# Kernel tuning notes

Measured on AMD Instinct MI355X. Metric: run time of the kernel, lower is better.

## Reference

```python
import jax, jax.numpy as jnp
import numpy as np

B, C, H, W, D = 4, 64, 64, 192, 24


def setup_inputs() -> dict:
    key = jax.random.key(0)
    ks = jax.random.split(key, 8)
    x = jax.random.normal(ks[0], (B, C, H, W), dtype=jnp.float32)
    y = jax.random.normal(ks[1], (B, C, H, W), dtype=jnp.float32)
    # disparity coordinate samples: pixel x-coordinates in [0, W-1]
    d1 = jax.random.uniform(ks[2], (B, D, H, W), dtype=jnp.float32) * (W - 1.0)
    d2 = jax.random.uniform(ks[3], (B, D, H, W), dtype=jnp.float32) * (W - 1.0)
    s = 1.0 / np.sqrt(C)
    qw = jax.random.normal(ks[4], (C, C), dtype=jnp.float32) * s
    qb = jax.random.normal(ks[5], (C,), dtype=jnp.float32) * 0.01
    kw = jax.random.normal(ks[6], (C, C), dtype=jnp.float32) * s
    kb = jax.random.normal(ks[7], (C,), dtype=jnp.float32) * 0.01
    return {"x": x, "y": y, "disp_range_samples1": d1, "disp_range_samples2": d2,
            "ndisp": D, "qw": qw, "qb": qb, "kw": kw, "kb": kb}


def _conv1x1(x, w, b):
    return jnp.einsum('oi,bihw->bohw', w, x) + b[None, :, None, None]


def _cost_volume(Q, K, disp_x):
    """mean_c( Q * grid_sample(K, bilinear, zeros, align_corners=False) ).
    Q,K: [B,C,H,W]; disp_x: [B,D,H,W] pixel x-coords. Returns [B,D,H,W]."""
    b, c, h, w = K.shape
    # torch grid_sample(align_corners=False) unnormalization of
    # coords = pix/((dim-1)/2)-1  ->  pix*dim/(dim-1) - 0.5
    xs = disp_x * (w / (w - 1.0)) - 0.5                      # [B,D,H,W]
    ys_row = jnp.arange(h, dtype=xs.dtype) * (h / (h - 1.0)) - 0.5
    ys = jnp.broadcast_to(ys_row[None, None, :, None], xs.shape)
    x0 = jnp.floor(xs)
    y0 = jnp.floor(ys)
    tx = xs - x0
    ty = ys - y0
    x0i = x0.astype(jnp.int32)
    y0i = y0.astype(jnp.int32)

    def corner(dy, dx, wgt):
        yi = y0i + dy
        xi = x0i + dx
        valid = ((yi >= 0) & (yi < h) & (xi >= 0) & (xi < w)).astype(Q.dtype)
        yc = jnp.clip(yi, 0, h - 1)
        xc = jnp.clip(xi, 0, w - 1)
        # per-batch gather: [C,H,W] indexed by [D,H,W] -> [C,D,H,W]
        g = jax.vmap(lambda im, yy, xx: im[:, yy, xx])(K, yc, xc)  # [B,C,D,H,W]
        return jnp.einsum('bchw,bcdhw->bdhw', Q, g * (wgt * valid)[:, None])

    cost = (corner(0, 0, (1.0 - ty) * (1.0 - tx)) +
            corner(0, 1, (1.0 - ty) * tx) +
            corner(1, 0, ty * (1.0 - tx)) +
            corner(1, 1, ty * tx))
    return cost / c


def reference(x, y, disp_range_samples1, disp_range_samples2, ndisp, qw, qb, kw, kb):
    assert ndisp == disp_range_samples1.shape[1]
    Q1 = _conv1x1(x, qw, qb)
    K1 = _conv1x1(y, kw, kb)
    cost1 = _cost_volume(Q1, K1, disp_range_samples1)
    Q2 = _conv1x1(y, qw, qb)
    K2 = _conv1x1(x, kw, kb)
    cost2 = _cost_volume(Q2, K2, disp_range_samples2)
    return (cost1, cost2)
```

## Files before the change

kernel.cpp:

```cpp
#include <hip/hip_runtime.h>
#include <stdint.h>

#define BB 4
#define CC 64
#define HH 64
#define WW 192
#define DD 24
#define HWQ (HH * WW)
#define PIX (BB * HWQ)

typedef __attribute__((ext_vector_type(8))) short short8;
typedef __attribute__((ext_vector_type(4))) float floatx4;

__device__ __forceinline__ float bf1(uint16_t u) {
    union { uint32_t i; float f; } c; c.i = ((uint32_t)u) << 16; return c.f;
}
__device__ __forceinline__ uint16_t f2bf(float f) {
    union { float f; uint32_t i; } c; c.f = f;
    uint32_t u = c.i;
    return (uint16_t)((u + 0x7fffu + ((u >> 16) & 1u)) >> 16);
}

#define A_SHORTS ((size_t)2 * PIX * CC)
#define S_F32OFF 4240

__global__ __launch_bounds__(64) void prep_kernel(
    const float* __restrict__ qw, const float* __restrict__ qb,
    const float* __restrict__ kw, const float* __restrict__ kb,
    float* __restrict__ fws) {
    const int bid = blockIdx.x;
    const int j   = threadIdx.x;
    if (bid < 64) {
        float acc = 0.f;
        for (int c = 0; c < CC; c++)
            acc = fmaf(qw[c * CC + bid], kw[c * CC + j], acc);
        fws[bid * 64 + j] = acc;
    } else if (bid == 64) {
        float bt = 0.f;
        for (int c = 0; c < CC; c++) bt = fmaf(qb[c], kw[c * CC + j], bt);
        fws[4096 + j] = bt;
        if (j == 0) {
            float g = 0.f;
            for (int c = 0; c < CC; c++) g = fmaf(qb[c], kb[c], g);
            fws[4224] = g;
        }
    } else {
        float al = 0.f;
        for (int c = 0; c < CC; c++) al = fmaf(qw[c * CC + j], kb[c], al);
        fws[4160 + j] = al;
    }
}

__global__ __launch_bounds__(256) void convA_kernel(
    const float* __restrict__ x, const float* __restrict__ y,
    const float* __restrict__ fws, uint16_t* __restrict__ A) {
    const int v = blockIdx.y;
    const float* src = v ? y : x;
    const float* G     = fws;
    const float* beta  = fws + 4096;
    const float* alpha = fws + 4160;
    const float* gamma = fws + 4224;
    float* s = const_cast<float*>(fws) + S_F32OFF;

    __shared__ float wt[64][64];
    __shared__ float bs[64], al[64];
    __shared__ float gm;
    const int tid = threadIdx.y * 64 + threadIdx.x;
    for (int idx = tid; idx < 4096; idx += 256) wt[idx >> 6][idx & 63] = G[idx];
    if (tid < 64) { bs[tid] = beta[tid]; al[tid] = alpha[tid]; }
    if (tid == 64) gm = *gamma;
    __syncthreads();

    const int pix0 = blockIdx.x * 256 + threadIdx.x * 4;
    const int b    = pix0 / HWQ;
    const int hw0  = pix0 - b * HWQ;
    const int j0   = threadIdx.y * 16;

    float acc[4][16];
#pragma unroll
    for (int p = 0; p < 4; p++)
#pragma unroll
        for (int k = 0; k < 16; k++) acc[p][k] = bs[j0 + k];
    float sac[4] = {gm, gm, gm, gm};

    const float* sp = src + (size_t)b * CC * HWQ + hw0;
#pragma unroll 4
    for (int i = 0; i < 64; i++) {
        float4 raw = *reinterpret_cast<const float4*>(sp + (size_t)i * HWQ);
        const float* wr = &wt[i][j0];
        const float av = al[i];
        sac[0] = fmaf(raw.x, av, sac[0]);
        sac[1] = fmaf(raw.y, av, sac[1]);
        sac[2] = fmaf(raw.z, av, sac[2]);
        sac[3] = fmaf(raw.w, av, sac[3]);
#pragma unroll
        for (int k = 0; k < 16; k++) {
            float wv = wr[k];
            acc[0][k] = fmaf(raw.x, wv, acc[0][k]);
            acc[1][k] = fmaf(raw.y, wv, acc[1][k]);
            acc[2][k] = fmaf(raw.z, wv, acc[2][k]);
            acc[3][k] = fmaf(raw.w, wv, acc[3][k]);
        }
    }

    uint16_t* dstv = A + (size_t)v * PIX * CC;
#pragma unroll
    for (int p = 0; p < 4; p++) {
        uint32_t pk[8];
#pragma unroll
        for (int k = 0; k < 8; k++)
            pk[k] = (uint32_t)f2bf(acc[p][2 * k]) | ((uint32_t)f2bf(acc[p][2 * k + 1]) << 16);
        uint16_t* dp = dstv + (size_t)(pix0 + p) * CC + j0;
        uint4 lo; lo.x = pk[0]; lo.y = pk[1]; lo.z = pk[2]; lo.w = pk[3];
        uint4 hi; hi.x = pk[4]; hi.y = pk[5]; hi.z = pk[6]; hi.w = pk[7];
        *reinterpret_cast<uint4*>(dp)     = lo;
        *reinterpret_cast<uint4*>(dp + 8) = hi;
    }
    if (threadIdx.y == 0) {
        float4 sv; sv.x = sac[0]; sv.y = sac[1]; sv.z = sac[2]; sv.w = sac[3];
        *reinterpret_cast<float4*>(s + (size_t)v * PIX + pix0) = sv;
    }
}

__global__ __launch_bounds__(256) void cost_kernel(
    const float* __restrict__ x, const float* __restrict__ y,
    const float* __restrict__ disp1, const float* __restrict__ disp2,
    const uint16_t* __restrict__ A, const float* __restrict__ fws,
    float* __restrict__ out) {
    const int h   = blockIdx.x;
    const int b   = blockIdx.y;
    const int v   = blockIdx.z >> 2;
    const int qtr = blockIdx.z & 3;
    const int w0  = qtr * 48;

    const float*    Yv   = v ? x : y;
    const float*    disp = v ? disp2 : disp1;
    const uint16_t* Ab   = A + ((size_t)v * PIX + (size_t)b * HWQ + h * WW + w0) * CC;
    const float*    sb   = fws + S_F32OFF + (size_t)v * PIX + (size_t)b * HWQ + h * WW + w0;

    const float ys  = (float)h * (float)(64.0 / 63.0) - 0.5f;
    const float y0f = floorf(ys);
    const float ty  = ys - y0f;
    const int   y0  = (int)y0f;
    const int   y1  = y0 + 1;
    const float vy0 = (y0 >= 0 && y0 < HH) ? 1.f : 0.f;
    const float vy1 = (y1 >= 0 && y1 < HH) ? 1.f : 0.f;
    const int   y0c = min(max(y0, 0), HH - 1);
    const int   y1c = min(max(y1, 0), HH - 1);
    const float ey0 = (1.f - ty) * vy0;
    const float ey1 = ty * vy1;
    const float eysum = ey0 + ey1;

    __shared__ uint16_t Yc[192 * 68];
    __shared__ uint16_t Pt[48 * 196];

    const int tid  = threadIdx.x;
    const int wave = tid >> 6;
    const int lane = tid & 63;
    const int lq   = lane >> 4;
    const int ln   = lane & 15;

    const uint16_t* ar0 = Ab + (size_t)ln * CC + lq * 8;
    short8 a0 = *reinterpret_cast<const short8*>(ar0);
    short8 a1 = *reinterpret_cast<const short8*>(ar0 + 32);

    const float* Yb0 = Yv + ((size_t)b * CC * HH + y0c) * WW;
    const float* Yb1 = Yv + ((size_t)b * CC * HH + y1c) * WW;
#pragma unroll
    for (int k = 0; k < 12; k++) {
        const int cg = wave + 4 * (k & 3);
        const int xx = (k >> 2) * 64 + lane;
        uint32_t pk[2];
#pragma unroll
        for (int half = 0; half < 2; half++) {
            uint32_t pv = 0;
#pragma unroll
            for (int j = 0; j < 2; j++) {
                const int c = cg * 4 + half * 2 + j;
                const float v0 = Yb0[(size_t)c * HH * WW + xx];
                const float v1 = Yb1[(size_t)c * HH * WW + xx];
                const float cb = fmaf(ey1, v1, ey0 * v0);
                pv |= ((uint32_t)f2bf(cb)) << (16 * j);
            }
            pk[half] = pv;
        }
        *reinterpret_cast<uint2*>(&Yc[xx * 68 + cg * 4]) = *reinterpret_cast<uint2*>(pk);
    }
    __syncthreads();

    for (int ch = 0; ch < 3; ch++) {
        short8 na0 = a0, na1 = a1;
        if (ch < 2) {
            const uint16_t* ar = Ab + (size_t)((ch + 1) * 16 + ln) * CC + lq * 8;
            na0 = *reinterpret_cast<const short8*>(ar);
            na1 = *reinterpret_cast<const short8*>(ar + 32);
        }
#pragma unroll
        for (int t3 = 0; t3 < 3; t3++) {
            const int Rb = (wave * 3 + t3) * 16;
            const uint16_t* yrow = &Yc[(Rb + ln) * 68 + lq * 8];
            short8 b0, b1;
            *reinterpret_cast<uint2*>(&b0)       = *reinterpret_cast<const uint2*>(yrow);
            *(reinterpret_cast<uint2*>(&b0) + 1) = *reinterpret_cast<const uint2*>(yrow + 4);
            *reinterpret_cast<uint2*>(&b1)       = *reinterpret_cast<const uint2*>(yrow + 32);
            *(reinterpret_cast<uint2*>(&b1) + 1) = *reinterpret_cast<const uint2*>(yrow + 36);
            floatx4 acc = {0.f, 0.f, 0.f, 0.f};
            acc = __builtin_amdgcn_mfma_f32_16x16x32_bf16(a0, b0, acc, 0, 0, 0);
            acc = __builtin_amdgcn_mfma_f32_16x16x32_bf16(a1, b1, acc, 0, 0, 0);
            const int pcol = Rb + ln;
            const int wl   = ch * 16 + lq * 4;
            Pt[(wl + 0) * 196 + pcol] = f2bf(acc[0]);
            Pt[(wl + 1) * 196 + pcol] = f2bf(acc[1]);
            Pt[(wl + 2) * 196 + pcol] = f2bf(acc[2]);
            Pt[(wl + 3) * 196 + pcol] = f2bf(acc[3]);
        }
        a0 = na0; a1 = na1;
    }
    __syncthreads();

    const float cx = (float)(192.0 / 191.0);
    const float inv_c = 1.f / 64.f;
    for (int o = tid; o < 48 * DD; o += 256) {
        const int wl = o % 48;
        const int d  = o / 48;
        const int w  = w0 + wl;
        const float dsv = disp[((size_t)(b * DD + d) * HH + h) * WW + w];
        const float xs  = dsv * cx - 0.5f;
        const float x0f = floorf(xs);
        const float tx  = xs - x0f;
        const int   x0  = (int)x0f;
        const int   x1  = x0 + 1;
        const float vx0 = (x0 >= 0 && x0 < WW) ? 1.f : 0.f;
        const float vx1 = (x1 >= 0 && x1 < WW) ? 1.f : 0.f;
        const int   x0c = min(max(x0, 0), WW - 1);
        const int   x1c = min(max(x1, 0), WW - 1);
        const float wx0 = (1.f - tx) * vx0;
        const float wx1 = tx * vx1;
        const float pc0 = bf1(Pt[wl * 196 + x0c]);
        const float pc1 = bf1(Pt[wl * 196 + x1c]);
        const float res = wx0 * pc0 + wx1 * pc1 + sb[wl] * (eysum * (wx0 + wx1));
        out[(((size_t)(v * BB + b) * DD + d) * HH + h) * WW + w] = res * inv_c;
    }
}

extern "C" void kernel_launch(void* const* d_in, const int* in_sizes, int n_in,
                              void* d_out, int out_size, void* d_ws, size_t ws_size,
                              hipStream_t stream) {
    const float* x  = (const float*)d_in[0];
    const float* y  = (const float*)d_in[1];
    const float* d1 = (const float*)d_in[2];
    const float* d2 = (const float*)d_in[3];
    const float* qw = (const float*)d_in[5];
    const float* qb = (const float*)d_in[6];
    const float* kw = (const float*)d_in[7];
    const float* kb = (const float*)d_in[8];

    uint16_t* A   = (uint16_t*)d_ws;
    float*    fws = (float*)((uint16_t*)d_ws + A_SHORTS);
    float*    out = (float*)d_out;

    prep_kernel<<<dim3(66), dim3(64), 0, stream>>>(qw, qb, kw, kb, fws);
    convA_kernel<<<dim3(PIX / 256, 2), dim3(64, 4), 0, stream>>>(x, y, fws, A);
    cost_kernel<<<dim3(HH, BB, 8), dim3(256), 0, stream>>>(x, y, d1, d2, A, fws, out);
}
```

Measured before the change: 138.5 us.

## Process full image row per block with 1024 threads to avoid redundant Yc builds

Each cost block now handles a whole row of 192 query pixels instead of a quarter, using 1024 threads and two halves of 96 pixels each. The bilinearly blended, bf16-packed K row (Yc) is built once per row instead of four times, which cuts the redundant global reads of the input row. The price is fewer, larger blocks (512 instead of 2048), a larger shared-memory tile, extra barriers, and only 12 of the 16 waves doing MFMA work, so occupancy and latency hiding may suffer.

```diff
diff --git a/kernel.cpp b/kernel.cpp
--- a/kernel.cpp
+++ b/kernel.cpp
@@ -122,21 +122,19 @@
     }
 }
 
-__global__ __launch_bounds__(256) void cost_kernel(
+__global__ __launch_bounds__(1024) void cost_kernel(
     const float* __restrict__ x, const float* __restrict__ y,
     const float* __restrict__ disp1, const float* __restrict__ disp2,
     const uint16_t* __restrict__ A, const float* __restrict__ fws,
     float* __restrict__ out) {
-    const int h   = blockIdx.x;
-    const int b   = blockIdx.y;
-    const int v   = blockIdx.z >> 2;
-    const int qtr = blockIdx.z & 3;
-    const int w0  = qtr * 48;
+    const int h = blockIdx.x;
+    const int b = blockIdx.y;
+    const int v = blockIdx.z;
 
     const float*    Yv   = v ? x : y;
     const float*    disp = v ? disp2 : disp1;
-    const uint16_t* Ab   = A + ((size_t)v * PIX + (size_t)b * HWQ + h * WW + w0) * CC;
-    const float*    sb   = fws + S_F32OFF + (size_t)v * PIX + (size_t)b * HWQ + h * WW + w0;
+    const uint16_t* Ab   = A + ((size_t)v * PIX + (size_t)b * HWQ + h * WW) * CC;
+    const float*    sb   = fws + S_F32OFF + (size_t)v * PIX + (size_t)b * HWQ + h * WW;
 
     const float ys  = (float)h * (float)(64.0 / 63.0) - 0.5f;
     const float y0f = floorf(ys);
@@ -152,7 +150,7 @@
     const float eysum = ey0 + ey1;
 
     __shared__ uint16_t Yc[192 * 68];
-    __shared__ uint16_t Pt[48 * 196];
+    __shared__ uint16_t Pt[96 * 196];
 
     const int tid  = threadIdx.x;
     const int wave = tid >> 6;
@@ -160,16 +158,12 @@
     const int lq   = lane >> 4;
     const int ln   = lane & 15;
 
-    const uint16_t* ar0 = Ab + (size_t)ln * CC + lq * 8;
-    short8 a0 = *reinterpret_cast<const short8*>(ar0);
-    short8 a1 = *reinterpret_cast<const short8*>(ar0 + 32);
-
     const float* Yb0 = Yv + ((size_t)b * CC * HH + y0c) * WW;
     const float* Yb1 = Yv + ((size_t)b * CC * HH + y1c) * WW;
 #pragma unroll
-    for (int k = 0; k < 12; k++) {
-        const int cg = wave + 4 * (k & 3);
-        const int xx = (k >> 2) * 64 + lane;
+    for (int k = 0; k < 3; k++) {
+        const int cg = wave;
+        const int xx = k * 64 + lane;
         uint32_t pk[2];
 #pragma unroll
         for (int half = 0; half < 2; half++) {
@@ -188,58 +182,60 @@
     }
     __syncthreads();
 
-    for (int ch = 0; ch < 3; ch++) {
-        short8 na0 = a0, na1 = a1;
-        if (ch < 2) {
-            const uint16_t* ar = Ab + (size_t)((ch + 1) * 16 + ln) * CC + lq * 8;
-            na0 = *reinterpret_cast<const short8*>(ar);
-            na1 = *reinterpret_cast<const short8*>(ar + 32);
-        }
-#pragma unroll
-        for (int t3 = 0; t3 < 3; t3++) {
-            const int Rb = (wave * 3 + t3) * 16;
-            const uint16_t* yrow = &Yc[(Rb + ln) * 68 + lq * 8];
-            short8 b0, b1;
-            *reinterpret_cast<uint2*>(&b0)       = *reinterpret_cast<const uint2*>(yrow);
-            *(reinterpret_cast<uint2*>(&b0) + 1) = *reinterpret_cast<const uint2*>(yrow + 4);
-            *reinterpret_cast<uint2*>(&b1)       = *reinterpret_cast<const uint2*>(yrow + 32);
-            *(reinterpret_cast<uint2*>(&b1) + 1) = *reinterpret_cast<const uint2*>(yrow + 36);
-            floatx4 acc = {0.f, 0.f, 0.f, 0.f};
-            acc = __builtin_amdgcn_mfma_f32_16x16x32_bf16(a0, b0, acc, 0, 0, 0);
-            acc = __builtin_amdgcn_mfma_f32_16x16x32_bf16(a1, b1, acc, 0, 0, 0);
-            const int pcol = Rb + ln;
-            const int wl   = ch * 16 + lq * 4;
-            Pt[(wl + 0) * 196 + pcol] = f2bf(acc[0]);
-            Pt[(wl + 1) * 196 + pcol] = f2bf(acc[1]);
-            Pt[(wl + 2) * 196 + pcol] = f2bf(acc[2]);
-            Pt[(wl + 3) * 196 + pcol] = f2bf(acc[3]);
-        }
-        a0 = na0; a1 = na1;
-    }
-    __syncthreads();
-
     const float cx = (float)(192.0 / 191.0);
     const float inv_c = 1.f / 64.f;
-    for (int o = tid; o < 48 * DD; o += 256) {
-        const int wl = o % 48;
-        const int d  = o / 48;
-        const int w  = w0 + wl;
-        const float dsv = disp[((size_t)(b * DD + d) * HH + h) * WW + w];
-        const float xs  = dsv * cx - 0.5f;
-        const float x0f = floorf(xs);
-        const float tx  = xs - x0f;
-        const int   x0  = (int)x0f;
-        const int   x1  = x0 + 1;
-        const float vx0 = (x0 >= 0 && x0 < WW) ? 1.f : 0.f;
-        const float vx1 = (x1 >= 0 && x1 < WW) ? 1.f : 0.f;
-        const int   x0c = min(max(x0, 0), WW - 1);
-        const int   x1c = min(max(x1, 0), WW - 1);
-        const float wx0 = (1.f - tx) * vx0;
-        const float wx1 = tx * vx1;
-        const float pc0 = bf1(Pt[wl * 196 + x0c]);
-        const float pc1 = bf1(Pt[wl * 196 + x1c]);
-        const float res = wx0 * pc0 + wx1 * pc1 + sb[wl] * (eysum * (wx0 + wx1));
-        out[(((size_t)(v * BB + b) * DD + d) * HH + h) * WW + w] = res * inv_c;
+
+    for (int half = 0; half < 2; half++) {
+        if (wave < 12) {
+            const int mcl = wave >> 1;
+            const uint16_t* ar = Ab + (size_t)(half * 96 + mcl * 16 + ln) * CC + lq * 8;
+            short8 a0 = *reinterpret_cast<const short8*>(ar);
+            short8 a1 = *reinterpret_cast<const short8*>(ar + 32);
+#pragma unroll
+            for (int i = 0; i < 6; i++) {
+                const int nt = (wave & 1) * 6 + i;
+                const int Rb = nt * 16;
+                const uint16_t* yrow = &Yc[(Rb + ln) * 68 + lq * 8];
+                short8 b0, b1;
+                *reinterpret_cast<uint2*>(&b0)       = *reinterpret_cast<const uint2*>(yrow);
+                *(reinterpret_cast<uint2*>(&b0) + 1) = *reinterpret_cast<const uint2*>(yrow + 4);
+                *reinterpret_cast<uint2*>(&b1)       = *reinterpret_cast<const uint2*>(yrow + 32);
+                *(reinterpret_cast<uint2*>(&b1) + 1) = *reinterpret_cast<const uint2*>(yrow + 36);
+                floatx4 acc = {0.f, 0.f, 0.f, 0.f};
+                acc = __builtin_amdgcn_mfma_f32_16x16x32_bf16(a0, b0, acc, 0, 0, 0);
+                acc = __builtin_amdgcn_mfma_f32_16x16x32_bf16(a1, b1, acc, 0, 0, 0);
+                const int pcol = Rb + ln;
+                const int wl   = mcl * 16 + lq * 4;
+                Pt[(wl + 0) * 196 + pcol] = f2bf(acc[0]);
+                Pt[(wl + 1) * 196 + pcol] = f2bf(acc[1]);
+                Pt[(wl + 2) * 196 + pcol] = f2bf(acc[2]);
+                Pt[(wl + 3) * 196 + pcol] = f2bf(acc[3]);
+            }
+        }
+        __syncthreads();
+
+        for (int o = tid; o < 96 * DD; o += 1024) {
+            const int wl = o % 96;
+            const int d  = o / 96;
+            const int w  = half * 96 + wl;
+            const float dsv = disp[((size_t)(b * DD + d) * HH + h) * WW + w];
+            const float xs  = dsv * cx - 0.5f;
+            const float x0f = floorf(xs);
+            const float tx  = xs - x0f;
+            const int   x0  = (int)x0f;
+            const int   x1  = x0 + 1;
+            const float vx0 = (x0 >= 0 && x0 < WW) ? 1.f : 0.f;
+            const float vx1 = (x1 >= 0 && x1 < WW) ? 1.f : 0.f;
+            const int   x0c = min(max(x0, 0), WW - 1);
+            const int   x1c = min(max(x1, 0), WW - 1);
+            const float wx0 = (1.f - tx) * vx0;
+            const float wx1 = tx * vx1;
+            const float pc0 = bf1(Pt[wl * 196 + x0c]);
+            const float pc1 = bf1(Pt[wl * 196 + x1c]);
+            const float res = wx0 * pc0 + wx1 * pc1 + sb[w] * (eysum * (wx0 + wx1));
+            out[(((size_t)(v * BB + b) * DD + d) * HH + h) * WW + w] = res * inv_c;
+        }
+        __syncthreads();
     }
 }
 
@@ -261,5 +257,5 @@
 
     prep_kernel<<<dim3(66), dim3(64), 0, stream>>>(qw, qb, kw, kb, fws);
     convA_kernel<<<dim3(PIX / 256, 2), dim3(64, 4), 0, stream>>>(x, y, fws, A);
-    cost_kernel<<<dim3(HH, BB, 8), dim3(256), 0, stream>>>(x, y, d1, d2, A, fws, out);
-}
+    cost_kernel<<<dim3(HH, BB, 2), dim3(1024), 0, stream>>>(x, y, d1, d2, A, fws, out);
+}
```

Measured after the change: 133.5 us. 1.04x faster.
